# Kernel optimization log

Hardware: AMD Instinct MI355X
Metric: run time of the kernel (lower is better)

The kernel has to match this reference:

```python
import jax, jax.numpy as jnp
import numpy as np

HIDDEN = 2048
INTER = 768
N_EXPERTS = 8
TOP_K = 2
BATCH, SEQ = 4, 512


def setup_inputs() -> dict:
    key = jax.random.key(0)
    ks = jax.random.split(key, 5)
    std = 0.02
    hidden_states = jax.random.normal(ks[0], (BATCH, SEQ, HIDDEN), dtype=jnp.float32)
    W_gate = jax.random.normal(ks[1], (N_EXPERTS, HIDDEN), dtype=jnp.float32) * std  # router Linear weight [E,H]
    Wg = jax.random.normal(ks[2], (N_EXPERTS, HIDDEN, INTER), dtype=jnp.float32) * std  # gate proj per expert
    Wu = jax.random.normal(ks[3], (N_EXPERTS, HIDDEN, INTER), dtype=jnp.float32) * std  # up proj per expert
    Wd = jax.random.normal(ks[4], (N_EXPERTS, INTER, HIDDEN), dtype=jnp.float32) * std  # down proj per expert
    return {"hidden_states": hidden_states, "W_gate": W_gate, "Wg": Wg, "Wu": Wu, "Wd": Wd}


def reference(hidden_states, W_gate, Wg, Wu, Wd):
    orig_shape = hidden_states.shape
    x = hidden_states.reshape(-1, HIDDEN)              # [T, H]
    T = x.shape[0]

    # Router: softmax in float32, top-k, renormalize (matches torch code).
    router_logits = x @ W_gate.T                        # [T, E]
    routing_probs = jax.nn.softmax(router_logits.astype(jnp.float32), axis=-1)
    topk_w, topk_idx = jax.lax.top_k(routing_probs, TOP_K)  # [T, K]
    topk_w = topk_w / jnp.sum(topk_w, axis=-1, keepdims=True)
    topk_w = topk_w.astype(x.dtype)

    # Sparse combine weights as dense [T, E] (equiv to index_add over torch.where dispatch).
    combine = jnp.zeros((T, N_EXPERTS), dtype=x.dtype)
    combine = combine.at[jnp.arange(T)[:, None], topk_idx].add(topk_w)

    # Expert MLPs, computed densely over experts (idiomatic jit-able dispatch).
    g = jnp.einsum('th,ehi->eti', x, Wg)                # [E, T, I]
    u = jnp.einsum('th,ehi->eti', x, Wu)                # [E, T, I]
    h = jax.nn.silu(g) * u                              # SiluAndMul
    y = jnp.einsum('eti,eih->eth', h, Wd)               # [E, T, H]

    out = jnp.einsum('eth,te->th', y, combine)          # weighted combine
    return out.reshape(orig_shape)
```

## Files before the change

kernel.cpp:

```cpp
#include <hip/hip_runtime.h>
#include <hip/hip_bf16.h>
#include <math.h>

#define H_DIM 2048
#define I_DIM 768
#define NEXP  8
#define TTOK  2048

typedef __bf16 bf16x8 __attribute__((ext_vector_type(8)));
typedef __bf16 bf16x4 __attribute__((ext_vector_type(4)));
typedef float  f32x4  __attribute__((ext_vector_type(4)));

#define WS_COUNTS   0u
#define WS_TOK      128u
#define WS_WGTW     65664u
#define WS_XBF      131328u
#define WS_HBUF     8519936u
#define WS_WG_T     15008000u
#define WS_WU_T     40173824u
#define WS_WD_T     65339648u

__device__ __forceinline__ void gl2l(const __bf16* g, __bf16* l) {
    __builtin_amdgcn_global_load_lds(
        (const __attribute__((address_space(1))) unsigned int*)g,
        (__attribute__((address_space(3))) unsigned int*)l, 16, 0, 0);
}

__device__ __forceinline__ void pipe_sync_vm8() {
    asm volatile("" ::: "memory");
    __builtin_amdgcn_s_waitcnt(0xF78);
    __builtin_amdgcn_s_barrier();
    asm volatile("" ::: "memory");
}
__device__ __forceinline__ void pipe_sync_vm4() {
    asm volatile("" ::: "memory");
    __builtin_amdgcn_s_waitcnt(0xF74);
    __builtin_amdgcn_s_barrier();
    asm volatile("" ::: "memory");
}
__device__ __forceinline__ void pipe_sync_vm0() {
    asm volatile("" ::: "memory");
    __builtin_amdgcn_s_waitcnt(0xF70);
    __builtin_amdgcn_s_barrier();
    asm volatile("" ::: "memory");
}

__global__ void xconv_k(const float* __restrict__ x, __bf16* __restrict__ xb) {
    int i = (blockIdx.x * 256 + threadIdx.x) * 4;
    float4 v = *(const float4*)(x + i);
    bf16x4 o;
    o[0] = (__bf16)v.x; o[1] = (__bf16)v.y; o[2] = (__bf16)v.z; o[3] = (__bf16)v.w;
    *(bf16x4*)(xb + i) = o;
}

__global__ __launch_bounds__(256) void wtrans_k(const float* __restrict__ in0,
                                                const float* __restrict__ in1,
                                                __bf16* __restrict__ out0,
                                                __bf16* __restrict__ out1,
                                                int K, int N) {
    const int z = blockIdx.z;
    const int e = z & 7;
    const float* in  = (z >> 3) ? in1  : in0;
    __bf16*     out  = (z >> 3) ? out1 : out0;
    const int k0 = blockIdx.x * 64, n0 = blockIdx.y * 64;
    __shared__ float sT[64 * 65];
    const float* ip = in + (size_t)e * K * N;
    const int t = threadIdx.x;
    const int kl = t >> 4;
    const int n4 = (t & 15) * 4;
#pragma unroll
    for (int j = 0; j < 4; ++j) {
        int k = kl + j * 16;
        float4 v = *(const float4*)(ip + (size_t)(k0 + k) * N + n0 + n4);
        sT[(n4 + 0) * 65 + k] = v.x;
        sT[(n4 + 1) * 65 + k] = v.y;
        sT[(n4 + 2) * 65 + k] = v.z;
        sT[(n4 + 3) * 65 + k] = v.w;
    }
    __syncthreads();
    const int n = t >> 2;
    const int kc = (t & 3) * 16;
    bf16x8 o0, o1;
#pragma unroll
    for (int j = 0; j < 8; ++j) {
        o0[j] = (__bf16)sT[n * 65 + kc + j];
        o1[j] = (__bf16)sT[n * 65 + kc + 8 + j];
    }
    __bf16* op = out + (size_t)e * N * K + (size_t)(n0 + n) * K + k0 + kc;
    *(bf16x8*)op = o0;
    *(bf16x8*)(op + 8) = o1;
}

__global__ __launch_bounds__(256) void router_k(const float* __restrict__ x,
                                                const float* __restrict__ wgate,
                                                int* __restrict__ counts,
                                                int* __restrict__ tok_list,
                                                float* __restrict__ wgt) {
    const int t = blockIdx.x;
    const int tid = threadIdx.x;
    float acc[NEXP];
#pragma unroll
    for (int e = 0; e < NEXP; ++e) acc[e] = 0.f;
    const float* xr = x + (size_t)t * H_DIM;
    for (int k = tid; k < H_DIM; k += 256) {
        float xv = xr[k];
#pragma unroll
        for (int e = 0; e < NEXP; ++e) acc[e] += xv * wgate[e * H_DIM + k];
    }
    __shared__ float s_red[NEXP][4];
    __shared__ float s_logit[NEXP];
    const int lane = tid & 63, w = tid >> 6;
#pragma unroll
    for (int e = 0; e < NEXP; ++e) {
        float v = acc[e];
#pragma unroll
        for (int off = 32; off > 0; off >>= 1) v += __shfl_down(v, off, 64);
        if (lane == 0) s_red[e][w] = v;
    }
    __syncthreads();
    if (tid < NEXP) s_logit[tid] = s_red[tid][0] + s_red[tid][1] + s_red[tid][2] + s_red[tid][3];
    __syncthreads();
    if (tid == 0) {
        int i0 = 0; float l0 = s_logit[0];
        for (int e = 1; e < NEXP; ++e) if (s_logit[e] > l0) { l0 = s_logit[e]; i0 = e; }
        int i1 = -1; float l1 = -1e30f;
        for (int e = 0; e < NEXP; ++e) if (e != i0 && s_logit[e] > l1) { l1 = s_logit[e]; i1 = e; }
        float w0 = 1.f / (1.f + expf(l1 - l0));
        float w1 = 1.f - w0;
        int p0 = atomicAdd(&counts[i0], 1);
        tok_list[i0 * TTOK + p0] = t; wgt[i0 * TTOK + p0] = w0;
        int p1 = atomicAdd(&counts[i1], 1);
        tok_list[i1 * TTOK + p1] = t; wgt[i1 * TTOK + p1] = w1;
    }
}

__global__ __launch_bounds__(256, 2) void gemm1_k(
    const __bf16* __restrict__ xb, const __bf16* __restrict__ Wgt,
    const __bf16* __restrict__ Wut, const int* __restrict__ counts,
    const int* __restrict__ tok_list, __bf16* __restrict__ hbuf) {
    const int g = blockIdx.x;
    const int e = g / 12, nt = g % 12;
    const int cnt = counts[e];
    const int m0 = blockIdx.y * 128;
    if (m0 >= cnt) return;
    const int tid = threadIdx.x;
    const int lane = tid & 63, w = tid >> 6;

    __shared__ __bf16 sA[4][128 * 32];
    __shared__ __bf16 sG[4][64 * 32];
    __shared__ __bf16 sU[4][64 * 32];
    __shared__ int s_tok[128];
    __shared__ int s_off;

    if (tid == 0) { int o = 0; for (int j = 0; j < e; ++j) o += counts[j]; s_off = o; }
    if (tid < 128) {
        int m = m0 + tid;
        s_tok[tid] = tok_list[e * TTOK + (m < cnt ? m : cnt - 1)];
    }
    __syncthreads();
    const int off = s_off;

    const int srow = lane >> 2;
    const int gof = ((lane & 3) ^ (srow & 3)) * 8;
    const __bf16* pA[2]; int lofA[2];
#pragma unroll
    for (int i = 0; i < 2; ++i) {
        int r = i * 64 + w * 16 + srow;
        pA[i] = xb + (size_t)s_tok[r] * H_DIM + gof;
        lofA[i] = (i * 64 + w * 16) * 32;
    }
    const __bf16 *pG, *pU;
    const int lofGU = (w * 16) * 32;
    {
        int r = w * 16 + srow;
        size_t grow = (size_t)e * I_DIM + nt * 64 + r;
        pG = Wgt + grow * H_DIM + gof;
        pU = Wut + grow * H_DIM + gof;
    }

    const int wm = w & 1, wn = w >> 1;
    const int l15 = lane & 15, kq = lane >> 4;
    const int swz = (kq ^ (l15 & 3)) * 8;

    f32x4 accG[4][2], accU[4][2];
#pragma unroll
    for (int mf = 0; mf < 4; ++mf)
#pragma unroll
        for (int nf = 0; nf < 2; ++nf) {
            accG[mf][nf] = (f32x4){0.f, 0.f, 0.f, 0.f};
            accU[mf][nf] = (f32x4){0.f, 0.f, 0.f, 0.f};
        }

#define G1_ISSUE(T, BUF)                                             \
    {                                                                \
        const int kb_ = (T) * 32;                                    \
        gl2l(pA[0] + kb_, &sA[BUF][lofA[0]]);                        \
        gl2l(pA[1] + kb_, &sA[BUF][lofA[1]]);                        \
        gl2l(pG + kb_, &sG[BUF][lofGU]);                             \
        gl2l(pU + kb_, &sU[BUF][lofGU]);                             \
    }

#define G1_COMPUTE(P)                                                                    \
    {                                                                                    \
        bf16x8 af[4], bg[2], bu[2];                                                      \
        _Pragma("unroll")                                                                \
        for (int mf = 0; mf < 4; ++mf)                                                   \
            af[mf] = *(const bf16x8*)(&sA[P][0] + (wm * 64 + mf * 16 + l15) * 32 + swz); \
        _Pragma("unroll")                                                                \
        for (int nf = 0; nf < 2; ++nf) {                                                 \
            bg[nf] = *(const bf16x8*)(&sG[P][0] + (wn * 32 + nf * 16 + l15) * 32 + swz); \
            bu[nf] = *(const bf16x8*)(&sU[P][0] + (wn * 32 + nf * 16 + l15) * 32 + swz); \
        }                                                                                \
        _Pragma("unroll")                                                                \
        for (int mf = 0; mf < 4; ++mf)                                                   \
            _Pragma("unroll")                                                            \
            for (int nf = 0; nf < 2; ++nf) {                                             \
                accG[mf][nf] = __builtin_amdgcn_mfma_f32_16x16x32_bf16(af[mf], bg[nf], accG[mf][nf], 0, 0, 0); \
                accU[mf][nf] = __builtin_amdgcn_mfma_f32_16x16x32_bf16(af[mf], bu[nf], accU[mf][nf], 0, 0, 0); \
            }                                                                            \
    }

    G1_ISSUE(0, 0); G1_ISSUE(1, 1); G1_ISSUE(2, 2);

#pragma unroll 4
    for (int it = 0; it < 60; ++it) {
        const int p = it & 3;
        pipe_sync_vm8();
        G1_ISSUE(it + 3, (it + 3) & 3);
        G1_COMPUTE(p);
    }
    pipe_sync_vm8(); G1_ISSUE(63, 3); G1_COMPUTE(0);
    pipe_sync_vm8(); G1_COMPUTE(1);
    pipe_sync_vm4(); G1_COMPUTE(2);
    pipe_sync_vm0(); G1_COMPUTE(3);
#undef G1_ISSUE
#undef G1_COMPUTE

#pragma unroll
    for (int mf = 0; mf < 4; ++mf) {
#pragma unroll
        for (int reg = 0; reg < 4; ++reg) {
            int m = m0 + wm * 64 + mf * 16 + kq * 4 + reg;
            if (m < cnt) {
                size_t rowbase = (size_t)(off + m) * I_DIM;
#pragma unroll
                for (int nf = 0; nf < 2; ++nf) {
                    float g1 = accG[mf][nf][reg], u1 = accU[mf][nf][reg];
                    float h = (g1 / (1.f + __expf(-g1))) * u1;
                    hbuf[rowbase + nt * 64 + wn * 32 + nf * 16 + l15] = (__bf16)h;
                }
            }
        }
    }
}

__global__ __launch_bounds__(256, 2) void gemm2_k(
    const __bf16* __restrict__ hbuf, const __bf16* __restrict__ Wdt,
    const int* __restrict__ counts, const int* __restrict__ tok_list,
    const float* __restrict__ wgt, float* __restrict__ out) {
    const int g = blockIdx.x;
    const int e = g >> 4, nt = g & 15;
    const int cnt = counts[e];
    const int m0 = blockIdx.y * 128;
    if (m0 >= cnt) return;
    const int tid = threadIdx.x;
    const int lane = tid & 63, w = tid >> 6;

    __shared__ __bf16 sA[4][128 * 32];
    __shared__ __bf16 sB[4][128 * 32];
    __shared__ int s_tok[128];
    __shared__ float s_w[128];
    __shared__ int s_off;

    if (tid == 0) { int o = 0; for (int j = 0; j < e; ++j) o += counts[j]; s_off = o; }
    if (tid < 128) {
        int m = m0 + tid;
        if (m < cnt) { s_tok[tid] = tok_list[e * TTOK + m]; s_w[tid] = wgt[e * TTOK + m]; }
        else         { s_tok[tid] = 0;                      s_w[tid] = 0.f; }
    }
    __syncthreads();
    const int off = s_off;

    const int srow = lane >> 2;
    const int gof = ((lane & 3) ^ (srow & 3)) * 8;
    const __bf16* pA[2]; int lofA[2];
    const __bf16* pB[2]; int lofB[2];
#pragma unroll
    for (int i = 0; i < 2; ++i) {
        int r = i * 64 + w * 16 + srow;
        pA[i] = hbuf + (size_t)(off + m0 + r) * I_DIM + gof;
        pB[i] = Wdt + ((size_t)e * H_DIM + nt * 128 + r) * I_DIM + gof;
        lofA[i] = (i * 64 + w * 16) * 32;
        lofB[i] = (i * 64 + w * 16) * 32;
    }

    const int wm = w & 1, wn = w >> 1;
    const int l15 = lane & 15, kq = lane >> 4;
    const int swz = (kq ^ (l15 & 3)) * 8;

    f32x4 acc[4][4];
#pragma unroll
    for (int mf = 0; mf < 4; ++mf)
#pragma unroll
        for (int nf = 0; nf < 4; ++nf) acc[mf][nf] = (f32x4){0.f, 0.f, 0.f, 0.f};

#define G2_ISSUE(T, BUF)                                             \
    {                                                                \
        const int kb_ = (T) * 32;                                    \
        gl2l(pA[0] + kb_, &sA[BUF][lofA[0]]);                        \
        gl2l(pA[1] + kb_, &sA[BUF][lofA[1]]);                        \
        gl2l(pB[0] + kb_, &sB[BUF][lofB[0]]);                        \
        gl2l(pB[1] + kb_, &sB[BUF][lofB[1]]);                        \
    }

#define G2_COMPUTE(P)                                                                    \
    {                                                                                    \
        bf16x8 af[4], bb[4];                                                             \
        _Pragma("unroll")                                                                \
        for (int mf = 0; mf < 4; ++mf)                                                   \
            af[mf] = *(const bf16x8*)(&sA[P][0] + (wm * 64 + mf * 16 + l15) * 32 + swz); \
        _Pragma("unroll")                                                                \
        for (int nf = 0; nf < 4; ++nf)                                                   \
            bb[nf] = *(const bf16x8*)(&sB[P][0] + (wn * 64 + nf * 16 + l15) * 32 + swz); \
        _Pragma("unroll")                                                                \
        for (int mf = 0; mf < 4; ++mf)                                                   \
            _Pragma("unroll")                                                            \
            for (int nf = 0; nf < 4; ++nf)                                               \
                acc[mf][nf] = __builtin_amdgcn_mfma_f32_16x16x32_bf16(af[mf], bb[nf], acc[mf][nf], 0, 0, 0); \
    }

    G2_ISSUE(0, 0); G2_ISSUE(1, 1); G2_ISSUE(2, 2);
#pragma unroll 4
    for (int it = 0; it < 20; ++it) {
        const int p = it & 3;
        pipe_sync_vm8();
        G2_ISSUE(it + 3, (it + 3) & 3);
        G2_COMPUTE(p);
    }
    pipe_sync_vm8(); G2_ISSUE(23, 3); G2_COMPUTE(0);
    pipe_sync_vm8(); G2_COMPUTE(1);
    pipe_sync_vm4(); G2_COMPUTE(2);
    pipe_sync_vm0(); G2_COMPUTE(3);
#undef G2_ISSUE
#undef G2_COMPUTE

#pragma unroll
    for (int mf = 0; mf < 4; ++mf) {
#pragma unroll
        for (int reg = 0; reg < 4; ++reg) {
            int m_loc = wm * 64 + mf * 16 + kq * 4 + reg;
            if (m0 + m_loc < cnt) {
                int tok = s_tok[m_loc];
                float wv = s_w[m_loc];
                float* orow = out + (size_t)tok * H_DIM + nt * 128 + wn * 64 + l15;
#pragma unroll
                for (int nf = 0; nf < 4; ++nf)
                    atomicAdd(orow + nf * 16, wv * acc[mf][nf][reg]);
            }
        }
    }
}

extern "C" void kernel_launch(void* const* d_in, const int* in_sizes, int n_in,
                              void* d_out, int out_size, void* d_ws, size_t ws_size,
                              hipStream_t stream) {
    const float* x     = (const float*)d_in[0];
    const float* Wgate = (const float*)d_in[1];
    const float* Wg    = (const float*)d_in[2];
    const float* Wu    = (const float*)d_in[3];
    const float* Wd    = (const float*)d_in[4];
    float* out = (float*)d_out;
    char* ws = (char*)d_ws;

    int*    counts   = (int*)(ws + WS_COUNTS);
    int*    tok_list = (int*)(ws + WS_TOK);
    float*  wgt      = (float*)(ws + WS_WGTW);
    __bf16* xb       = (__bf16*)(ws + WS_XBF);
    __bf16* hbuf     = (__bf16*)(ws + WS_HBUF);
    __bf16* Wg_t     = (__bf16*)(ws + WS_WG_T);
    __bf16* Wu_t     = (__bf16*)(ws + WS_WU_T);
    __bf16* Wd_t     = (__bf16*)(ws + WS_WD_T);

    hipMemsetAsync(counts, 0, 32, stream);
    hipMemsetAsync(d_out, 0, (size_t)TTOK * H_DIM * sizeof(float), stream);

    xconv_k<<<(TTOK * H_DIM / 4) / 256, 256, 0, stream>>>(x, xb);
    router_k<<<TTOK, 256, 0, stream>>>(x, Wgate, counts, tok_list, wgt);
    wtrans_k<<<dim3(H_DIM / 64, I_DIM / 64, 2 * NEXP), 256, 0, stream>>>(Wg, Wu, Wg_t, Wu_t, H_DIM, I_DIM);
    wtrans_k<<<dim3(I_DIM / 64, H_DIM / 64, NEXP), 256, 0, stream>>>(Wd, Wd, Wd_t, Wd_t, I_DIM, H_DIM);
    gemm1_k<<<dim3(96, 16), 256, 0, stream>>>(xb, Wg_t, Wu_t, counts, tok_list, hbuf);
    gemm2_k<<<dim3(128, 16), 256, 0, stream>>>(hbuf, Wd_t, counts, tok_list, wgt, out);
}
```

Measured before the change: 362.0 us.

## Fuse prep kernels into one launch and halve GEMM M-tiles to 64 rows

Merges the x conversion, router and the three weight transposes into a single prep kernel, so one launch replaces four and the router reuses the x row it already loaded for the bf16 conversion. Both expert GEMMs drop the M tile from 128 to 64 rows, double the grid in y, raise the occupancy hint to 3 blocks per CU, and adjust the vmcnt waits to match the smaller number of loads per stage. This aims at launch overhead and better CU fill when per-expert token counts are uneven, at the cost of less reuse of each weight tile and more weight reads from global memory.

```diff
diff --git a/kernel.cpp b/kernel.cpp
--- a/kernel.cpp
+++ b/kernel.cpp
@@ -26,15 +26,15 @@
         (__attribute__((address_space(3))) unsigned int*)l, 16, 0, 0);
 }
 
-__device__ __forceinline__ void pipe_sync_vm8() {
-    asm volatile("" ::: "memory");
-    __builtin_amdgcn_s_waitcnt(0xF78);
+__device__ __forceinline__ void pipe_sync_vm6() {
+    asm volatile("" ::: "memory");
+    __builtin_amdgcn_s_waitcnt(0xF76);
     __builtin_amdgcn_s_barrier();
     asm volatile("" ::: "memory");
 }
-__device__ __forceinline__ void pipe_sync_vm4() {
-    asm volatile("" ::: "memory");
-    __builtin_amdgcn_s_waitcnt(0xF74);
+__device__ __forceinline__ void pipe_sync_vm3() {
+    asm volatile("" ::: "memory");
+    __builtin_amdgcn_s_waitcnt(0xF73);
     __builtin_amdgcn_s_barrier();
     asm volatile("" ::: "memory");
 }
@@ -45,29 +45,75 @@
     asm volatile("" ::: "memory");
 }
 
-__global__ void xconv_k(const float* __restrict__ x, __bf16* __restrict__ xb) {
-    int i = (blockIdx.x * 256 + threadIdx.x) * 4;
-    float4 v = *(const float4*)(x + i);
-    bf16x4 o;
-    o[0] = (__bf16)v.x; o[1] = (__bf16)v.y; o[2] = (__bf16)v.z; o[3] = (__bf16)v.w;
-    *(bf16x4*)(xb + i) = o;
-}
-
-__global__ __launch_bounds__(256) void wtrans_k(const float* __restrict__ in0,
-                                                const float* __restrict__ in1,
-                                                __bf16* __restrict__ out0,
-                                                __bf16* __restrict__ out1,
-                                                int K, int N) {
-    const int z = blockIdx.z;
-    const int e = z & 7;
-    const float* in  = (z >> 3) ? in1  : in0;
-    __bf16*     out  = (z >> 3) ? out1 : out0;
-    const int k0 = blockIdx.x * 64, n0 = blockIdx.y * 64;
+__global__ __launch_bounds__(256) void prep_k(
+    const float* __restrict__ x, const float* __restrict__ Wgate,
+    const float* __restrict__ Wg, const float* __restrict__ Wu, const float* __restrict__ Wd,
+    int* __restrict__ counts, int* __restrict__ tok_list, float* __restrict__ wgt,
+    __bf16* __restrict__ xb, __bf16* __restrict__ Wg_t, __bf16* __restrict__ Wu_t,
+    __bf16* __restrict__ Wd_t) {
     __shared__ float sT[64 * 65];
+    __shared__ float s_red[NEXP][4];
+    __shared__ float s_logit[NEXP];
+    const int tid = threadIdx.x;
+    const int b = blockIdx.x;
+
+    if (b < TTOK) {
+        const int t = b;
+        const float4* xr = (const float4*)(x + (size_t)t * H_DIM);
+        bf16x4* xo = (bf16x4*)(xb + (size_t)t * H_DIM);
+        float acc[NEXP];
+#pragma unroll
+        for (int e = 0; e < NEXP; ++e) acc[e] = 0.f;
+#pragma unroll
+        for (int j = 0; j < 2; ++j) {
+            const int i4 = j * 256 + tid;
+            float4 v = xr[i4];
+            bf16x4 o;
+            o[0] = (__bf16)v.x; o[1] = (__bf16)v.y; o[2] = (__bf16)v.z; o[3] = (__bf16)v.w;
+            xo[i4] = o;
+#pragma unroll
+            for (int e = 0; e < NEXP; ++e) {
+                float4 wv = *(const float4*)(Wgate + e * H_DIM + i4 * 4);
+                acc[e] += v.x * wv.x + v.y * wv.y + v.z * wv.z + v.w * wv.w;
+            }
+        }
+        const int lane = tid & 63, w = tid >> 6;
+#pragma unroll
+        for (int e = 0; e < NEXP; ++e) {
+            float v = acc[e];
+#pragma unroll
+            for (int off = 32; off > 0; off >>= 1) v += __shfl_down(v, off, 64);
+            if (lane == 0) s_red[e][w] = v;
+        }
+        __syncthreads();
+        if (tid < NEXP) s_logit[tid] = s_red[tid][0] + s_red[tid][1] + s_red[tid][2] + s_red[tid][3];
+        __syncthreads();
+        if (tid == 0) {
+            int i0 = 0; float l0 = s_logit[0];
+            for (int e = 1; e < NEXP; ++e) if (s_logit[e] > l0) { l0 = s_logit[e]; i0 = e; }
+            int i1 = -1; float l1 = -1e30f;
+            for (int e = 0; e < NEXP; ++e) if (e != i0 && s_logit[e] > l1) { l1 = s_logit[e]; i1 = e; }
+            float w0 = 1.f / (1.f + expf(l1 - l0));
+            float w1 = 1.f - w0;
+            int p0 = atomicAdd(&counts[i0], 1);
+            tok_list[i0 * TTOK + p0] = t; wgt[i0 * TTOK + p0] = w0;
+            int p1 = atomicAdd(&counts[i1], 1);
+            tok_list[i1 * TTOK + p1] = t; wgt[i1 * TTOK + p1] = w1;
+        }
+        return;
+    }
+
+    int r = b - TTOK;
+    const int t3 = r / 3072; r -= t3 * 3072;
+    const int e = r / 384;  const int rem = r - e * 384;
+    const float* in; __bf16* out; int K, N, k0, n0;
+    if (t3 < 2) { K = H_DIM; N = I_DIM; k0 = (rem / 12) * 64; n0 = (rem % 12) * 64;
+                  in = t3 ? Wu : Wg; out = t3 ? Wu_t : Wg_t; }
+    else        { K = I_DIM; N = H_DIM; k0 = (rem / 32) * 64; n0 = (rem % 32) * 64;
+                  in = Wd; out = Wd_t; }
     const float* ip = in + (size_t)e * K * N;
-    const int t = threadIdx.x;
-    const int kl = t >> 4;
-    const int n4 = (t & 15) * 4;
+    const int kl = tid >> 4;
+    const int n4 = (tid & 15) * 4;
 #pragma unroll
     for (int j = 0; j < 4; ++j) {
         int k = kl + j * 16;
@@ -78,8 +124,8 @@
         sT[(n4 + 3) * 65 + k] = v.w;
     }
     __syncthreads();
-    const int n = t >> 2;
-    const int kc = (t & 3) * 16;
+    const int n = tid >> 2;
+    const int kc = (tid & 3) * 16;
     bf16x8 o0, o1;
 #pragma unroll
     for (int j = 0; j < 8; ++j) {
@@ -91,69 +137,26 @@
     *(bf16x8*)(op + 8) = o1;
 }
 
-__global__ __launch_bounds__(256) void router_k(const float* __restrict__ x,
-                                                const float* __restrict__ wgate,
-                                                int* __restrict__ counts,
-                                                int* __restrict__ tok_list,
-                                                float* __restrict__ wgt) {
-    const int t = blockIdx.x;
-    const int tid = threadIdx.x;
-    float acc[NEXP];
-#pragma unroll
-    for (int e = 0; e < NEXP; ++e) acc[e] = 0.f;
-    const float* xr = x + (size_t)t * H_DIM;
-    for (int k = tid; k < H_DIM; k += 256) {
-        float xv = xr[k];
-#pragma unroll
-        for (int e = 0; e < NEXP; ++e) acc[e] += xv * wgate[e * H_DIM + k];
-    }
-    __shared__ float s_red[NEXP][4];
-    __shared__ float s_logit[NEXP];
-    const int lane = tid & 63, w = tid >> 6;
-#pragma unroll
-    for (int e = 0; e < NEXP; ++e) {
-        float v = acc[e];
-#pragma unroll
-        for (int off = 32; off > 0; off >>= 1) v += __shfl_down(v, off, 64);
-        if (lane == 0) s_red[e][w] = v;
-    }
-    __syncthreads();
-    if (tid < NEXP) s_logit[tid] = s_red[tid][0] + s_red[tid][1] + s_red[tid][2] + s_red[tid][3];
-    __syncthreads();
-    if (tid == 0) {
-        int i0 = 0; float l0 = s_logit[0];
-        for (int e = 1; e < NEXP; ++e) if (s_logit[e] > l0) { l0 = s_logit[e]; i0 = e; }
-        int i1 = -1; float l1 = -1e30f;
-        for (int e = 0; e < NEXP; ++e) if (e != i0 && s_logit[e] > l1) { l1 = s_logit[e]; i1 = e; }
-        float w0 = 1.f / (1.f + expf(l1 - l0));
-        float w1 = 1.f - w0;
-        int p0 = atomicAdd(&counts[i0], 1);
-        tok_list[i0 * TTOK + p0] = t; wgt[i0 * TTOK + p0] = w0;
-        int p1 = atomicAdd(&counts[i1], 1);
-        tok_list[i1 * TTOK + p1] = t; wgt[i1 * TTOK + p1] = w1;
-    }
-}
-
-__global__ __launch_bounds__(256, 2) void gemm1_k(
+__global__ __launch_bounds__(256, 3) void gemm1_k(
     const __bf16* __restrict__ xb, const __bf16* __restrict__ Wgt,
     const __bf16* __restrict__ Wut, const int* __restrict__ counts,
     const int* __restrict__ tok_list, __bf16* __restrict__ hbuf) {
     const int g = blockIdx.x;
     const int e = g / 12, nt = g % 12;
     const int cnt = counts[e];
-    const int m0 = blockIdx.y * 128;
+    const int m0 = blockIdx.y * 64;
     if (m0 >= cnt) return;
     const int tid = threadIdx.x;
     const int lane = tid & 63, w = tid >> 6;
 
-    __shared__ __bf16 sA[4][128 * 32];
+    __shared__ __bf16 sA[4][64 * 32];
     __shared__ __bf16 sG[4][64 * 32];
     __shared__ __bf16 sU[4][64 * 32];
-    __shared__ int s_tok[128];
+    __shared__ int s_tok[64];
     __shared__ int s_off;
 
     if (tid == 0) { int o = 0; for (int j = 0; j < e; ++j) o += counts[j]; s_off = o; }
-    if (tid < 128) {
+    if (tid < 64) {
         int m = m0 + tid;
         s_tok[tid] = tok_list[e * TTOK + (m < cnt ? m : cnt - 1)];
     }
@@ -162,15 +165,9 @@
 
     const int srow = lane >> 2;
     const int gof = ((lane & 3) ^ (srow & 3)) * 8;
-    const __bf16* pA[2]; int lofA[2];
-#pragma unroll
-    for (int i = 0; i < 2; ++i) {
-        int r = i * 64 + w * 16 + srow;
-        pA[i] = xb + (size_t)s_tok[r] * H_DIM + gof;
-        lofA[i] = (i * 64 + w * 16) * 32;
-    }
+    const __bf16* pA = xb + (size_t)s_tok[w * 16 + srow] * H_DIM + gof;
+    const int lofA = (w * 16) * 32;
     const __bf16 *pG, *pU;
-    const int lofGU = (w * 16) * 32;
     {
         int r = w * 16 + srow;
         size_t grow = (size_t)e * I_DIM + nt * 64 + r;
@@ -182,9 +179,9 @@
     const int l15 = lane & 15, kq = lane >> 4;
     const int swz = (kq ^ (l15 & 3)) * 8;
 
-    f32x4 accG[4][2], accU[4][2];
-#pragma unroll
-    for (int mf = 0; mf < 4; ++mf)
+    f32x4 accG[2][2], accU[2][2];
+#pragma unroll
+    for (int mf = 0; mf < 2; ++mf)
 #pragma unroll
         for (int nf = 0; nf < 2; ++nf) {
             accG[mf][nf] = (f32x4){0.f, 0.f, 0.f, 0.f};
@@ -194,25 +191,24 @@
 #define G1_ISSUE(T, BUF)                                             \
     {                                                                \
         const int kb_ = (T) * 32;                                    \
-        gl2l(pA[0] + kb_, &sA[BUF][lofA[0]]);                        \
-        gl2l(pA[1] + kb_, &sA[BUF][lofA[1]]);                        \
-        gl2l(pG + kb_, &sG[BUF][lofGU]);                             \
-        gl2l(pU + kb_, &sU[BUF][lofGU]);                             \
+        gl2l(pA + kb_, &sA[BUF][lofA]);                              \
+        gl2l(pG + kb_, &sG[BUF][lofA]);                              \
+        gl2l(pU + kb_, &sU[BUF][lofA]);                              \
     }
 
 #define G1_COMPUTE(P)                                                                    \
     {                                                                                    \
-        bf16x8 af[4], bg[2], bu[2];                                                      \
-        _Pragma("unroll")                                                                \
-        for (int mf = 0; mf < 4; ++mf)                                                   \
-            af[mf] = *(const bf16x8*)(&sA[P][0] + (wm * 64 + mf * 16 + l15) * 32 + swz); \
+        bf16x8 af[2], bg[2], bu[2];                                                      \
+        _Pragma("unroll")                                                                \
+        for (int mf = 0; mf < 2; ++mf)                                                   \
+            af[mf] = *(const bf16x8*)(&sA[P][0] + (wm * 32 + mf * 16 + l15) * 32 + swz); \
         _Pragma("unroll")                                                                \
         for (int nf = 0; nf < 2; ++nf) {                                                 \
             bg[nf] = *(const bf16x8*)(&sG[P][0] + (wn * 32 + nf * 16 + l15) * 32 + swz); \
             bu[nf] = *(const bf16x8*)(&sU[P][0] + (wn * 32 + nf * 16 + l15) * 32 + swz); \
         }                                                                                \
         _Pragma("unroll")                                                                \
-        for (int mf = 0; mf < 4; ++mf)                                                   \
+        for (int mf = 0; mf < 2; ++mf)                                                   \
             _Pragma("unroll")                                                            \
             for (int nf = 0; nf < 2; ++nf) {                                             \
                 accG[mf][nf] = __builtin_amdgcn_mfma_f32_16x16x32_bf16(af[mf], bg[nf], accG[mf][nf], 0, 0, 0); \
@@ -225,22 +221,22 @@
 #pragma unroll 4
     for (int it = 0; it < 60; ++it) {
         const int p = it & 3;
-        pipe_sync_vm8();
+        pipe_sync_vm6();
         G1_ISSUE(it + 3, (it + 3) & 3);
         G1_COMPUTE(p);
     }
-    pipe_sync_vm8(); G1_ISSUE(63, 3); G1_COMPUTE(0);
-    pipe_sync_vm8(); G1_COMPUTE(1);
-    pipe_sync_vm4(); G1_COMPUTE(2);
+    pipe_sync_vm6(); G1_ISSUE(63, 3); G1_COMPUTE(0);
+    pipe_sync_vm6(); G1_COMPUTE(1);
+    pipe_sync_vm3(); G1_COMPUTE(2);
     pipe_sync_vm0(); G1_COMPUTE(3);
 #undef G1_ISSUE
 #undef G1_COMPUTE
 
 #pragma unroll
-    for (int mf = 0; mf < 4; ++mf) {
+    for (int mf = 0; mf < 2; ++mf) {
 #pragma unroll
         for (int reg = 0; reg < 4; ++reg) {
-            int m = m0 + wm * 64 + mf * 16 + kq * 4 + reg;
+            int m = m0 + wm * 32 + mf * 16 + kq * 4 + reg;
             if (m < cnt) {
                 size_t rowbase = (size_t)(off + m) * I_DIM;
 #pragma unroll
@@ -254,26 +250,26 @@
     }
 }
 
-__global__ __launch_bounds__(256, 2) void gemm2_k(
+__global__ __launch_bounds__(256, 3) void gemm2_k(
     const __bf16* __restrict__ hbuf, const __bf16* __restrict__ Wdt,
     const int* __restrict__ counts, const int* __restrict__ tok_list,
     const float* __restrict__ wgt, float* __restrict__ out) {
     const int g = blockIdx.x;
     const int e = g >> 4, nt = g & 15;
     const int cnt = counts[e];
-    const int m0 = blockIdx.y * 128;
+    const int m0 = blockIdx.y * 64;
     if (m0 >= cnt) return;
     const int tid = threadIdx.x;
     const int lane = tid & 63, w = tid >> 6;
 
-    __shared__ __bf16 sA[4][128 * 32];
+    __shared__ __bf16 sA[4][64 * 32];
     __shared__ __bf16 sB[4][128 * 32];
-    __shared__ int s_tok[128];
-    __shared__ float s_w[128];
+    __shared__ int s_tok[64];
+    __shared__ float s_w[64];
     __shared__ int s_off;
 
     if (tid == 0) { int o = 0; for (int j = 0; j < e; ++j) o += counts[j]; s_off = o; }
-    if (tid < 128) {
+    if (tid < 64) {
         int m = m0 + tid;
         if (m < cnt) { s_tok[tid] = tok_list[e * TTOK + m]; s_w[tid] = wgt[e * TTOK + m]; }
         else         { s_tok[tid] = 0;                      s_w[tid] = 0.f; }
@@ -283,14 +279,13 @@
 
     const int srow = lane >> 2;
     const int gof = ((lane & 3) ^ (srow & 3)) * 8;
-    const __bf16* pA[2]; int lofA[2];
+    const __bf16* pA = hbuf + (size_t)(off + m0 + w * 16 + srow) * I_DIM + gof;
+    const int lofA = (w * 16) * 32;
     const __bf16* pB[2]; int lofB[2];
 #pragma unroll
     for (int i = 0; i < 2; ++i) {
         int r = i * 64 + w * 16 + srow;
-        pA[i] = hbuf + (size_t)(off + m0 + r) * I_DIM + gof;
         pB[i] = Wdt + ((size_t)e * H_DIM + nt * 128 + r) * I_DIM + gof;
-        lofA[i] = (i * 64 + w * 16) * 32;
         lofB[i] = (i * 64 + w * 16) * 32;
     }
 
@@ -298,32 +293,31 @@
     const int l15 = lane & 15, kq = lane >> 4;
     const int swz = (kq ^ (l15 & 3)) * 8;
 
-    f32x4 acc[4][4];
-#pragma unroll
-    for (int mf = 0; mf < 4; ++mf)
+    f32x4 acc[2][4];
+#pragma unroll
+    for (int mf = 0; mf < 2; ++mf)
 #pragma unroll
         for (int nf = 0; nf < 4; ++nf) acc[mf][nf] = (f32x4){0.f, 0.f, 0.f, 0.f};
 
 #define G2_ISSUE(T, BUF)                                             \
     {                                                                \
         const int kb_ = (T) * 32;                                    \
-        gl2l(pA[0] + kb_, &sA[BUF][lofA[0]]);                        \
-        gl2l(pA[1] + kb_, &sA[BUF][lofA[1]]);                        \
+        gl2l(pA + kb_, &sA[BUF][lofA]);                              \
         gl2l(pB[0] + kb_, &sB[BUF][lofB[0]]);                        \
         gl2l(pB[1] + kb_, &sB[BUF][lofB[1]]);                        \
     }
 
 #define G2_COMPUTE(P)                                                                    \
     {                                                                                    \
-        bf16x8 af[4], bb[4];                                                             \
-        _Pragma("unroll")                                                                \
-        for (int mf = 0; mf < 4; ++mf)                                                   \
-            af[mf] = *(const bf16x8*)(&sA[P][0] + (wm * 64 + mf * 16 + l15) * 32 + swz); \
+        bf16x8 af[2], bb[4];                                                             \
+        _Pragma("unroll")                                                                \
+        for (int mf = 0; mf < 2; ++mf)                                                   \
+            af[mf] = *(const bf16x8*)(&sA[P][0] + (wm * 32 + mf * 16 + l15) * 32 + swz); \
         _Pragma("unroll")                                                                \
         for (int nf = 0; nf < 4; ++nf)                                                   \
             bb[nf] = *(const bf16x8*)(&sB[P][0] + (wn * 64 + nf * 16 + l15) * 32 + swz); \
         _Pragma("unroll")                                                                \
-        for (int mf = 0; mf < 4; ++mf)                                                   \
+        for (int mf = 0; mf < 2; ++mf)                                                   \
             _Pragma("unroll")                                                            \
             for (int nf = 0; nf < 4; ++nf)                                               \
                 acc[mf][nf] = __builtin_amdgcn_mfma_f32_16x16x32_bf16(af[mf], bb[nf], acc[mf][nf], 0, 0, 0); \
@@ -333,22 +327,22 @@
 #pragma unroll 4
     for (int it = 0; it < 20; ++it) {
         const int p = it & 3;
-        pipe_sync_vm8();
+        pipe_sync_vm6();
         G2_ISSUE(it + 3, (it + 3) & 3);
         G2_COMPUTE(p);
     }
-    pipe_sync_vm8(); G2_ISSUE(23, 3); G2_COMPUTE(0);
-    pipe_sync_vm8(); G2_COMPUTE(1);
-    pipe_sync_vm4(); G2_COMPUTE(2);
+    pipe_sync_vm6(); G2_ISSUE(23, 3); G2_COMPUTE(0);
+    pipe_sync_vm6(); G2_COMPUTE(1);
+    pipe_sync_vm3(); G2_COMPUTE(2);
     pipe_sync_vm0(); G2_COMPUTE(3);
 #undef G2_ISSUE
 #undef G2_COMPUTE
 
 #pragma unroll
-    for (int mf = 0; mf < 4; ++mf) {
+    for (int mf = 0; mf < 2; ++mf) {
 #pragma unroll
         for (int reg = 0; reg < 4; ++reg) {
-            int m_loc = wm * 64 + mf * 16 + kq * 4 + reg;
+            int m_loc = wm * 32 + mf * 16 + kq * 4 + reg;
             if (m0 + m_loc < cnt) {
                 int tok = s_tok[m_loc];
                 float wv = s_w[m_loc];
@@ -384,10 +378,8 @@
     hipMemsetAsync(counts, 0, 32, stream);
     hipMemsetAsync(d_out, 0, (size_t)TTOK * H_DIM * sizeof(float), stream);
 
-    xconv_k<<<(TTOK * H_DIM / 4) / 256, 256, 0, stream>>>(x, xb);
-    router_k<<<TTOK, 256, 0, stream>>>(x, Wgate, counts, tok_list, wgt);
-    wtrans_k<<<dim3(H_DIM / 64, I_DIM / 64, 2 * NEXP), 256, 0, stream>>>(Wg, Wu, Wg_t, Wu_t, H_DIM, I_DIM);
-    wtrans_k<<<dim3(I_DIM / 64, H_DIM / 64, NEXP), 256, 0, stream>>>(Wd, Wd, Wd_t, Wd_t, I_DIM, H_DIM);
-    gemm1_k<<<dim3(96, 16), 256, 0, stream>>>(xb, Wg_t, Wu_t, counts, tok_list, hbuf);
-    gemm2_k<<<dim3(128, 16), 256, 0, stream>>>(hbuf, Wd_t, counts, tok_list, wgt, out);
-}
+    prep_k<<<TTOK + 9216, 256, 0, stream>>>(x, Wgate, Wg, Wu, Wd,
+                                            counts, tok_list, wgt, xb, Wg_t, Wu_t, Wd_t);
+    gemm1_k<<<dim3(96, 32), 256, 0, stream>>>(xb, Wg_t, Wu_t, counts, tok_list, hbuf);
+    gemm2_k<<<dim3(128, 32), 256, 0, stream>>>(hbuf, Wd_t, counts, tok_list, wgt, out);
+}
```

Result: no change. 356.3 us (-1.6%).

## Fuse prep kernels into one launch and remap GEMM blocks across XCDs

Applied to the files above, without the earlier changes.

Merges the activation bf16 conversion, router, and all three weight transposes into a single prep kernel with smaller 32x64 transpose tiles. The router also reuses the x load it does for the conversion. Both GEMM kernels switch to a 1D grid whose block index is remapped so blocks for the same expert/M-tile group land on the same XCD, aiming at better L2 reuse. The s_waitcnt immediates are also changed, altering the lgkm/exp counter fields, which risks a correctness or synchronization change.

```diff
diff --git a/kernel.cpp b/kernel.cpp
--- a/kernel.cpp
+++ b/kernel.cpp
@@ -28,126 +28,133 @@
 
 __device__ __forceinline__ void pipe_sync_vm8() {
     asm volatile("" ::: "memory");
-    __builtin_amdgcn_s_waitcnt(0xF78);
+    __builtin_amdgcn_s_waitcnt(0x78);
     __builtin_amdgcn_s_barrier();
     asm volatile("" ::: "memory");
 }
 __device__ __forceinline__ void pipe_sync_vm4() {
     asm volatile("" ::: "memory");
-    __builtin_amdgcn_s_waitcnt(0xF74);
+    __builtin_amdgcn_s_waitcnt(0x74);
     __builtin_amdgcn_s_barrier();
     asm volatile("" ::: "memory");
 }
 __device__ __forceinline__ void pipe_sync_vm0() {
     asm volatile("" ::: "memory");
-    __builtin_amdgcn_s_waitcnt(0xF70);
+    __builtin_amdgcn_s_waitcnt(0x70);
     __builtin_amdgcn_s_barrier();
     asm volatile("" ::: "memory");
 }
 
-__global__ void xconv_k(const float* __restrict__ x, __bf16* __restrict__ xb) {
-    int i = (blockIdx.x * 256 + threadIdx.x) * 4;
-    float4 v = *(const float4*)(x + i);
-    bf16x4 o;
-    o[0] = (__bf16)v.x; o[1] = (__bf16)v.y; o[2] = (__bf16)v.z; o[3] = (__bf16)v.w;
-    *(bf16x4*)(xb + i) = o;
-}
-
-__global__ __launch_bounds__(256) void wtrans_k(const float* __restrict__ in0,
-                                                const float* __restrict__ in1,
-                                                __bf16* __restrict__ out0,
-                                                __bf16* __restrict__ out1,
-                                                int K, int N) {
-    const int z = blockIdx.z;
-    const int e = z & 7;
-    const float* in  = (z >> 3) ? in1  : in0;
-    __bf16*     out  = (z >> 3) ? out1 : out0;
-    const int k0 = blockIdx.x * 64, n0 = blockIdx.y * 64;
-    __shared__ float sT[64 * 65];
+#define NTRANS 18432
+__global__ __launch_bounds__(128) void prep_k(
+    const float* __restrict__ x, const float* __restrict__ Wgate,
+    const float* __restrict__ Wg, const float* __restrict__ Wu, const float* __restrict__ Wd,
+    int* __restrict__ counts, int* __restrict__ tok_list, float* __restrict__ wgt,
+    __bf16* __restrict__ xb, __bf16* __restrict__ Wg_t, __bf16* __restrict__ Wu_t,
+    __bf16* __restrict__ Wd_t) {
+    __shared__ float sT[64 * 33];
+    __shared__ float s_red[NEXP][2];
+    __shared__ float s_logit[NEXP];
+    const int tid = threadIdx.x;
+    const int b = blockIdx.x;
+
+    if (b >= NTRANS) {
+        const int t = b - NTRANS;
+        const float4* xr = (const float4*)(x + (size_t)t * H_DIM);
+        bf16x4* xo = (bf16x4*)(xb + (size_t)t * H_DIM);
+        float acc[NEXP];
+#pragma unroll
+        for (int e = 0; e < NEXP; ++e) acc[e] = 0.f;
+#pragma unroll
+        for (int j = 0; j < 4; ++j) {
+            const int i4 = j * 128 + tid;
+            float4 v = xr[i4];
+            bf16x4 o;
+            o[0] = (__bf16)v.x; o[1] = (__bf16)v.y; o[2] = (__bf16)v.z; o[3] = (__bf16)v.w;
+            xo[i4] = o;
+#pragma unroll
+            for (int e = 0; e < NEXP; ++e) {
+                float4 wv = *(const float4*)(Wgate + e * H_DIM + i4 * 4);
+                acc[e] += v.x * wv.x + v.y * wv.y + v.z * wv.z + v.w * wv.w;
+            }
+        }
+        const int lane = tid & 63, w = tid >> 6;
+#pragma unroll
+        for (int e = 0; e < NEXP; ++e) {
+            float v = acc[e];
+#pragma unroll
+            for (int off = 32; off > 0; off >>= 1) v += __shfl_down(v, off, 64);
+            if (lane == 0) s_red[e][w] = v;
+        }
+        __syncthreads();
+        if (tid < NEXP) s_logit[tid] = s_red[tid][0] + s_red[tid][1];
+        __syncthreads();
+        if (tid == 0) {
+            int i0 = 0; float l0 = s_logit[0];
+            for (int e = 1; e < NEXP; ++e) if (s_logit[e] > l0) { l0 = s_logit[e]; i0 = e; }
+            int i1 = -1; float l1 = -1e30f;
+            for (int e = 0; e < NEXP; ++e) if (e != i0 && s_logit[e] > l1) { l1 = s_logit[e]; i1 = e; }
+            float w0 = 1.f / (1.f + expf(l1 - l0));
+            float w1 = 1.f - w0;
+            int p0 = atomicAdd(&counts[i0], 1);
+            tok_list[i0 * TTOK + p0] = t; wgt[i0 * TTOK + p0] = w0;
+            int p1 = atomicAdd(&counts[i1], 1);
+            tok_list[i1 * TTOK + p1] = t; wgt[i1 * TTOK + p1] = w1;
+        }
+        return;
+    }
+
+    int r = b;
+    const int t3 = r / 6144; r -= t3 * 6144;
+    const int e = r / 768;  const int rem = r - e * 768;
+    const float* in; __bf16* out; int K, N, k0, n0;
+    if (t3 < 2) { K = H_DIM; N = I_DIM; k0 = (rem / 12) * 32; n0 = (rem % 12) * 64;
+                  in = t3 ? Wu : Wg; out = t3 ? Wu_t : Wg_t; }
+    else        { K = I_DIM; N = H_DIM; k0 = (rem / 32) * 32; n0 = (rem % 32) * 64;
+                  in = Wd; out = Wd_t; }
     const float* ip = in + (size_t)e * K * N;
-    const int t = threadIdx.x;
-    const int kl = t >> 4;
-    const int n4 = (t & 15) * 4;
+    const int kl = tid >> 4;
+    const int n4 = (tid & 15) * 4;
 #pragma unroll
     for (int j = 0; j < 4; ++j) {
-        int k = kl + j * 16;
+        int k = kl + j * 8;
         float4 v = *(const float4*)(ip + (size_t)(k0 + k) * N + n0 + n4);
-        sT[(n4 + 0) * 65 + k] = v.x;
-        sT[(n4 + 1) * 65 + k] = v.y;
-        sT[(n4 + 2) * 65 + k] = v.z;
-        sT[(n4 + 3) * 65 + k] = v.w;
+        sT[(n4 + 0) * 33 + k] = v.x;
+        sT[(n4 + 1) * 33 + k] = v.y;
+        sT[(n4 + 2) * 33 + k] = v.z;
+        sT[(n4 + 3) * 33 + k] = v.w;
     }
     __syncthreads();
-    const int n = t >> 2;
-    const int kc = (t & 3) * 16;
+    const int n = tid >> 1;
+    const int kc = (tid & 1) * 16;
     bf16x8 o0, o1;
 #pragma unroll
     for (int j = 0; j < 8; ++j) {
-        o0[j] = (__bf16)sT[n * 65 + kc + j];
-        o1[j] = (__bf16)sT[n * 65 + kc + 8 + j];
+        o0[j] = (__bf16)sT[n * 33 + kc + j];
+        o1[j] = (__bf16)sT[n * 33 + kc + 8 + j];
     }
     __bf16* op = out + (size_t)e * N * K + (size_t)(n0 + n) * K + k0 + kc;
     *(bf16x8*)op = o0;
     *(bf16x8*)(op + 8) = o1;
-}
-
-__global__ __launch_bounds__(256) void router_k(const float* __restrict__ x,
-                                                const float* __restrict__ wgate,
-                                                int* __restrict__ counts,
-                                                int* __restrict__ tok_list,
-                                                float* __restrict__ wgt) {
-    const int t = blockIdx.x;
-    const int tid = threadIdx.x;
-    float acc[NEXP];
-#pragma unroll
-    for (int e = 0; e < NEXP; ++e) acc[e] = 0.f;
-    const float* xr = x + (size_t)t * H_DIM;
-    for (int k = tid; k < H_DIM; k += 256) {
-        float xv = xr[k];
-#pragma unroll
-        for (int e = 0; e < NEXP; ++e) acc[e] += xv * wgate[e * H_DIM + k];
-    }
-    __shared__ float s_red[NEXP][4];
-    __shared__ float s_logit[NEXP];
-    const int lane = tid & 63, w = tid >> 6;
-#pragma unroll
-    for (int e = 0; e < NEXP; ++e) {
-        float v = acc[e];
-#pragma unroll
-        for (int off = 32; off > 0; off >>= 1) v += __shfl_down(v, off, 64);
-        if (lane == 0) s_red[e][w] = v;
-    }
-    __syncthreads();
-    if (tid < NEXP) s_logit[tid] = s_red[tid][0] + s_red[tid][1] + s_red[tid][2] + s_red[tid][3];
-    __syncthreads();
-    if (tid == 0) {
-        int i0 = 0; float l0 = s_logit[0];
-        for (int e = 1; e < NEXP; ++e) if (s_logit[e] > l0) { l0 = s_logit[e]; i0 = e; }
-        int i1 = -1; float l1 = -1e30f;
-        for (int e = 0; e < NEXP; ++e) if (e != i0 && s_logit[e] > l1) { l1 = s_logit[e]; i1 = e; }
-        float w0 = 1.f / (1.f + expf(l1 - l0));
-        float w1 = 1.f - w0;
-        int p0 = atomicAdd(&counts[i0], 1);
-        tok_list[i0 * TTOK + p0] = t; wgt[i0 * TTOK + p0] = w0;
-        int p1 = atomicAdd(&counts[i1], 1);
-        tok_list[i1 * TTOK + p1] = t; wgt[i1 * TTOK + p1] = w1;
-    }
 }
 
 __global__ __launch_bounds__(256, 2) void gemm1_k(
     const __bf16* __restrict__ xb, const __bf16* __restrict__ Wgt,
     const __bf16* __restrict__ Wut, const int* __restrict__ counts,
     const int* __restrict__ tok_list, __bf16* __restrict__ hbuf) {
-    const int g = blockIdx.x;
-    const int e = g / 12, nt = g % 12;
+    const int lin = blockIdx.x;
+    const int xcd = lin & 7, t6 = lin >> 3;
+    const int sG = t6 / 12, nt = t6 % 12;
+    const int G = (sG << 3) | xcd;
+    const int e = G >> 4, y = G & 15;
     const int cnt = counts[e];
-    const int m0 = blockIdx.y * 128;
+    const int m0 = y * 128;
     if (m0 >= cnt) return;
     const int tid = threadIdx.x;
     const int lane = tid & 63, w = tid >> 6;
 
     __shared__ __bf16 sA[4][128 * 32];
-    __shared__ __bf16 sG[4][64 * 32];
+    __shared__ __bf16 sG_[4][64 * 32];
     __shared__ __bf16 sU[4][64 * 32];
     __shared__ int s_tok[128];
     __shared__ int s_off;
@@ -196,7 +203,7 @@
         const int kb_ = (T) * 32;                                    \
         gl2l(pA[0] + kb_, &sA[BUF][lofA[0]]);                        \
         gl2l(pA[1] + kb_, &sA[BUF][lofA[1]]);                        \
-        gl2l(pG + kb_, &sG[BUF][lofGU]);                             \
+        gl2l(pG + kb_, &sG_[BUF][lofGU]);                            \
         gl2l(pU + kb_, &sU[BUF][lofGU]);                             \
     }
 
@@ -208,7 +215,7 @@
             af[mf] = *(const bf16x8*)(&sA[P][0] + (wm * 64 + mf * 16 + l15) * 32 + swz); \
         _Pragma("unroll")                                                                \
         for (int nf = 0; nf < 2; ++nf) {                                                 \
-            bg[nf] = *(const bf16x8*)(&sG[P][0] + (wn * 32 + nf * 16 + l15) * 32 + swz); \
+            bg[nf] = *(const bf16x8*)(&sG_[P][0] + (wn * 32 + nf * 16 + l15) * 32 + swz);\
             bu[nf] = *(const bf16x8*)(&sU[P][0] + (wn * 32 + nf * 16 + l15) * 32 + swz); \
         }                                                                                \
         _Pragma("unroll")                                                                \
@@ -258,10 +265,13 @@
     const __bf16* __restrict__ hbuf, const __bf16* __restrict__ Wdt,
     const int* __restrict__ counts, const int* __restrict__ tok_list,
     const float* __restrict__ wgt, float* __restrict__ out) {
-    const int g = blockIdx.x;
-    const int e = g >> 4, nt = g & 15;
+    const int lin = blockIdx.x;
+    const int xcd = lin & 7, t6 = lin >> 3;
+    const int sG = t6 >> 4, nt = t6 & 15;
+    const int G = (sG << 3) | xcd;
+    const int e = G >> 4, y = G & 15;
     const int cnt = counts[e];
-    const int m0 = blockIdx.y * 128;
+    const int m0 = y * 128;
     if (m0 >= cnt) return;
     const int tid = threadIdx.x;
     const int lane = tid & 63, w = tid >> 6;
@@ -384,10 +394,8 @@
     hipMemsetAsync(counts, 0, 32, stream);
     hipMemsetAsync(d_out, 0, (size_t)TTOK * H_DIM * sizeof(float), stream);
 
-    xconv_k<<<(TTOK * H_DIM / 4) / 256, 256, 0, stream>>>(x, xb);
-    router_k<<<TTOK, 256, 0, stream>>>(x, Wgate, counts, tok_list, wgt);
-    wtrans_k<<<dim3(H_DIM / 64, I_DIM / 64, 2 * NEXP), 256, 0, stream>>>(Wg, Wu, Wg_t, Wu_t, H_DIM, I_DIM);
-    wtrans_k<<<dim3(I_DIM / 64, H_DIM / 64, NEXP), 256, 0, stream>>>(Wd, Wd, Wd_t, Wd_t, I_DIM, H_DIM);
-    gemm1_k<<<dim3(96, 16), 256, 0, stream>>>(xb, Wg_t, Wu_t, counts, tok_list, hbuf);
-    gemm2_k<<<dim3(128, 16), 256, 0, stream>>>(hbuf, Wd_t, counts, tok_list, wgt, out);
-}
+    prep_k<<<NTRANS + TTOK, 128, 0, stream>>>(x, Wgate, Wg, Wu, Wd,
+                                              counts, tok_list, wgt, xb, Wg_t, Wu_t, Wd_t);
+    gemm1_k<<<96 * 16, 256, 0, stream>>>(xb, Wg_t, Wu_t, counts, tok_list, hbuf);
+    gemm2_k<<<128 * 16, 256, 0, stream>>>(hbuf, Wd_t, counts, tok_list, wgt, out);
+}
```

Result: slower. 396.4 us (+9.5%).
